# Performance work log

Measured on AMD Instinct MI355X. Metric: run time of the kernel, lower is better.

## Reference

```python
import jax, jax.numpy as jnp
import numpy as np

N = 50000
E = 1600000
D_IN, D_EMB, D_H, D_OUT, HEADS = 128, 128, 128, 64, 2


def setup_inputs() -> dict:
    key = jax.random.key(0)
    ks = jax.random.split(key, 12)
    return {
        "x": jax.random.normal(ks[0], (N, D_IN), jnp.float32),
        "edge_index": jax.random.randint(ks[1], (2, E), 0, N, dtype=jnp.int32),
        "node_indices": jnp.arange(N, dtype=jnp.int32),
        "emb": jax.random.normal(ks[2], (N, D_EMB), jnp.float32) * 0.1,
        "W_gcn": jax.random.normal(ks[3], (D_IN + D_EMB, D_H), jnp.float32) * 0.06,
        "b_gcn": jnp.zeros((D_H,), jnp.float32),
        "W_sage_l": jax.random.normal(ks[4], (D_H, D_H), jnp.float32) * 0.08,
        "W_sage_r": jax.random.normal(ks[5], (D_H, D_H), jnp.float32) * 0.08,
        "b_sage": jnp.zeros((D_H,), jnp.float32),
        "W_gat": jax.random.normal(ks[6], (D_H, HEADS, D_H), jnp.float32) * 0.08,
        "att_src": jax.random.normal(ks[7], (HEADS, D_H), jnp.float32) * 0.1,
        "att_dst": jax.random.normal(ks[8], (HEADS, D_H), jnp.float32) * 0.1,
        "b_gat": jnp.zeros((D_H,), jnp.float32),
        "W_out": jax.random.normal(ks[9], (D_H, D_OUT), jnp.float32) * 0.08,
        "b_out": jnp.zeros((D_OUT,), jnp.float32),
    }


def _forward(x, edge_index, node_indices, emb, W_gcn, b_gcn,
             W_sage_l, W_sage_r, b_sage, W_gat, att_src, att_dst, b_gat,
             W_out, b_out):
    n = x.shape[0]
    seg = jax.ops.segment_sum
    loops = jnp.arange(n, dtype=edge_index.dtype)

    # node2vec embedding lookup + concat
    h = jnp.concatenate([x, emb[node_indices]], axis=1)  # [N, D_IN+D_EMB]

    # --- GCNConv (symmetric norm, self loops) ---
    src = jnp.concatenate([edge_index[0], loops])
    dst = jnp.concatenate([edge_index[1], loops])
    deg = seg(jnp.ones_like(dst, jnp.float32), dst, num_segments=n)
    dinv = jnp.where(deg > 0, jax.lax.rsqrt(jnp.maximum(deg, 1.0)), 0.0)
    norm = dinv[src] * dinv[dst]                     # [E+N]
    hW = h @ W_gcn                                   # [N, D_H]
    h = seg(hW[src] * norm[:, None], dst, num_segments=n) + b_gcn
    h = jax.nn.relu(h)

    # --- SAGEConv (mean aggregation, no self loops) ---
    s, d = edge_index[0], edge_index[1]
    agg = seg(h[s], d, num_segments=n)
    cnt = seg(jnp.ones_like(d, jnp.float32), d, num_segments=n)
    mean = agg / jnp.maximum(cnt, 1.0)[:, None]
    h = mean @ W_sage_l + h @ W_sage_r + b_sage
    h = jax.nn.relu(h)

    # --- GATConv heads=2, concat=False (mean over heads), self loops ---
    xW = jnp.einsum('nd,dhc->nhc', h, W_gat)         # [N, H, D_H]
    a_src = jnp.einsum('nhc,hc->nh', xW, att_src)    # [N, H]
    a_dst = jnp.einsum('nhc,hc->nh', xW, att_dst)
    alpha = jax.nn.leaky_relu(a_src[src] + a_dst[dst], 0.2)  # [E+N, H]
    amax = jax.ops.segment_max(alpha, dst, num_segments=n)
    alpha = jnp.exp(alpha - amax[dst])
    asum = seg(alpha, dst, num_segments=n)
    alpha = alpha / (asum[dst] + 1e-16)
    out = seg(xW[src] * alpha[:, :, None], dst, num_segments=n)  # [N, H, D_H]
    h = jax.nn.relu(out.mean(axis=1) + b_gat)

    return h @ W_out + b_out


def reference(x, edge_index, node_indices, emb, W_gcn, b_gcn,
              W_sage_l, W_sage_r, b_sage, W_gat, att_src, att_dst, b_gat,
              W_out, b_out):
    return _forward(x, edge_index, node_indices, emb, W_gcn, b_gcn,
                    W_sage_l, W_sage_r, b_sage, W_gat, att_src, att_dst, b_gat,
                    W_out, b_out)
```

## Files before the change

### kernel.cpp

```cpp
#include <hip/hip_runtime.h>


typedef short bf16x8 __attribute__((ext_vector_type(8)));
typedef float f32x4  __attribute__((ext_vector_type(4)));

static __device__ __forceinline__ float leaky02(float x) {
    return x > 0.f ? x : 0.2f * x;
}
static __device__ __forceinline__ unsigned short f2bf(float f) {
    unsigned u = __float_as_uint(f);
    u = (u + 0x7FFFu + ((u >> 16) & 1u)) >> 16;
    return (unsigned short)u;
}
static __device__ __forceinline__ float bf2f(unsigned short h) {
    return __uint_as_float(((unsigned)h) << 16);
}
static __device__ __forceinline__ float4 bf4(ushort4 h) {
    return make_float4(bf2f(h.x), bf2f(h.y), bf2f(h.z), bf2f(h.w));
}
static __device__ __forceinline__ void split_bf(float v, unsigned short& h,
                                                unsigned short& l) {
    unsigned u = __float_as_uint(v);
    unsigned uh = u & 0xFFFF0000u;
    h = (unsigned short)(uh >> 16);
    l = f2bf(v - __uint_as_float(uh));
}

__global__ void deg_edges(const int* __restrict__ dst, int* __restrict__ degi, int E) {
    int e = blockIdx.x * blockDim.x + threadIdx.x;
    if (e < E) atomicAdd(&degi[dst[e]], 1);
}

__global__ __launch_bounds__(256)
void scan_part_norm(const int* __restrict__ degi, int* __restrict__ partial,
                    float* __restrict__ dinv, float* __restrict__ icnt, int n)
{
    int t = threadIdx.x;
    int base = blockIdx.x * 1024 + t * 4;
    int s = 0;
#pragma unroll
    for (int i = 0; i < 4; ++i) {
        int g = base + i;
        if (g < n) {
            int de = degi[g];
            s += de;
            dinv[g] = rsqrtf((float)(de + 1));
            icnt[g] = 1.0f / (float)(de > 1 ? de : 1);
        }
    }
#pragma unroll
    for (int m = 32; m > 0; m >>= 1) s += __shfl_xor(s, m, 64);
    __shared__ int wsum[4];
    if ((t & 63) == 0) wsum[t >> 6] = s;
    __syncthreads();
    if (t == 0) partial[blockIdx.x] = wsum[0] + wsum[1] + wsum[2] + wsum[3];
}

__global__ __launch_bounds__(64)
void scan_offsets(int* __restrict__ partial, int nb)
{
    int t = threadIdx.x;
    int carry = 0;
    for (int base = 0; base < nb; base += 64) {
        int i = base + t;
        int v = (i < nb) ? partial[i] : 0;
        int incl = v;
#pragma unroll
        for (int m = 1; m < 64; m <<= 1) {
            int o = __shfl_up(incl, m, 64);
            if (t >= m) incl += o;
        }
        if (i < nb) partial[i] = incl - v + carry;
        carry += __shfl(incl, 63, 64);
    }
}

__global__ __launch_bounds__(256)
void scan_write(const int* __restrict__ degi, const int* __restrict__ partial,
                int* __restrict__ rowptr, int n)
{
    __shared__ int tmp[256];
    int t = threadIdx.x;
    int base = blockIdx.x * 1024 + t * 4;
    int v[4]; int s = 0;
#pragma unroll
    for (int i = 0; i < 4; ++i) {
        int g = base + i;
        v[i] = (g < n) ? degi[g] : 0;
        s += v[i];
    }
    tmp[t] = s;
    __syncthreads();
    for (int off = 1; off < 256; off <<= 1) {
        int a = (t >= off) ? tmp[t - off] : 0;
        __syncthreads();
        tmp[t] += a;
        __syncthreads();
    }
    int run = tmp[t] - s + partial[blockIdx.x];
#pragma unroll
    for (int i = 0; i < 4; ++i) {
        int g = base + i;
        run += v[i];
        if (g < n) rowptr[g + 1] = run;
    }
    if (blockIdx.x == 0 && t == 0) rowptr[0] = 0;
}

__global__ void csr_fill(const int* __restrict__ src, const int* __restrict__ dst,
                         const int* __restrict__ rowptr, int* __restrict__ fill,
                         int* __restrict__ csr, int E)
{
    int e = blockIdx.x * blockDim.x + threadIdx.x;
    if (e >= E) return;
    int d = dst[e];
    int pos = rowptr[d] + atomicAdd(&fill[d], 1);
    csr[pos] = src[e];
}

template<bool HAS_A2, bool RELU, bool HAS_BIAS, bool HAS_IDX, bool SCALE,
         bool ATT, bool OUT_BF16>
__global__ __launch_bounds__(256)
void gemm_mfma(const float* __restrict__ A1, const float* __restrict__ W1,
               const float* __restrict__ A2, const float* __restrict__ W2,
               const int* __restrict__ idx2, const float* __restrict__ bias,
               const float* __restrict__ scale,
               const float* __restrict__ att_src, const float* __restrict__ att_dst,
               float* __restrict__ a_s, float* __restrict__ a_d,
               float* __restrict__ C, int nrows, int ncW, int ncC)
{
    __shared__ unsigned short ABh[8][65][8], ABl[8][65][8];
    __shared__ unsigned short WBh[8][65][8], WBl[8][65][8];
    const int t    = threadIdx.x;
    const int lane = t & 63;
    const int wv   = t >> 6;
    const int l15  = lane & 15;
    const int lg   = lane >> 4;
    const int row0 = blockIdx.x * 128;
    const int colOff = blockIdx.y * 128;

    f32x4 acc[2][8];
#pragma unroll
    for (int mt = 0; mt < 2; ++mt)
#pragma unroll
        for (int nt = 0; nt < 8; ++nt) acc[mt][nt] = (f32x4){0.f, 0.f, 0.f, 0.f};

    const int npass = HAS_A2 ? 2 : 1;
    for (int p = 0; p < npass; ++p) {
        const float* A = (p == 0) ? A1 : A2;
        const float* W = (p == 0) ? W1 : W2;
        for (int kt = 0; kt < 4; ++kt) {
#pragma unroll
            for (int i = 0; i < 4; ++i) {
                int f = i * 256 + t;
                int r = f >> 3, c4 = (f & 7) << 2;
                int row = row0 + r; if (row >= nrows) row = nrows - 1;
                int arow = (p == 1 && HAS_IDX) ? idx2[row] : row;
                float4 v = *(const float4*)(A + (size_t)arow * 128 + kt * 32 + c4);
                int rg = r >> 4;
                int slot = (r & 15) + ((c4 >> 3) << 4);
                int joff = c4 & 4;
                unsigned short h0,l0,h1,l1,h2,l2,h3,l3;
                split_bf(v.x, h0, l0); split_bf(v.y, h1, l1);
                split_bf(v.z, h2, l2); split_bf(v.w, h3, l3);
                *(ushort4*)&ABh[rg][slot][joff] = make_ushort4(h0, h1, h2, h3);
                *(ushort4*)&ABl[rg][slot][joff] = make_ushort4(l0, l1, l2, l3);
            }
#pragma unroll
            for (int i = 0; i < 4; ++i) {
                int f = i * 256 + t;
                int wr = f >> 5, wc4 = (f & 31) << 2;
                float4 v = *(const float4*)(W + (size_t)(kt * 32 + wr) * ncW + colOff + wc4);
                int jj = wr & 7, kg16 = (wr >> 3) << 4;
                int nt = wc4 >> 4, sb = (wc4 & 15) + kg16;
                unsigned short h, l;
                split_bf(v.x, h, l); WBh[nt][sb + 0][jj] = h; WBl[nt][sb + 0][jj] = l;
                split_bf(v.y, h, l); WBh[nt][sb + 1][jj] = h; WBl[nt][sb + 1][jj] = l;
                split_bf(v.z, h, l); WBh[nt][sb + 2][jj] = h; WBl[nt][sb + 2][jj] = l;
                split_bf(v.w, h, l); WBh[nt][sb + 3][jj] = h; WBl[nt][sb + 3][jj] = l;
            }
            __syncthreads();
            bf16x8 ah0 = *reinterpret_cast<const bf16x8*>(&ABh[wv * 2 + 0][lane][0]);
            bf16x8 al0 = *reinterpret_cast<const bf16x8*>(&ABl[wv * 2 + 0][lane][0]);
            bf16x8 ah1 = *reinterpret_cast<const bf16x8*>(&ABh[wv * 2 + 1][lane][0]);
            bf16x8 al1 = *reinterpret_cast<const bf16x8*>(&ABl[wv * 2 + 1][lane][0]);
#pragma unroll
            for (int nt = 0; nt < 8; ++nt) {
                bf16x8 bh = *reinterpret_cast<const bf16x8*>(&WBh[nt][lane][0]);
                bf16x8 bl = *reinterpret_cast<const bf16x8*>(&WBl[nt][lane][0]);
                acc[0][nt] = __builtin_amdgcn_mfma_f32_16x16x32_bf16(al0, bh, acc[0][nt], 0, 0, 0);
                acc[0][nt] = __builtin_amdgcn_mfma_f32_16x16x32_bf16(ah0, bl, acc[0][nt], 0, 0, 0);
                acc[0][nt] = __builtin_amdgcn_mfma_f32_16x16x32_bf16(ah0, bh, acc[0][nt], 0, 0, 0);
                acc[1][nt] = __builtin_amdgcn_mfma_f32_16x16x32_bf16(al1, bh, acc[1][nt], 0, 0, 0);
                acc[1][nt] = __builtin_amdgcn_mfma_f32_16x16x32_bf16(ah1, bl, acc[1][nt], 0, 0, 0);
                acc[1][nt] = __builtin_amdgcn_mfma_f32_16x16x32_bf16(ah1, bh, acc[1][nt], 0, 0, 0);
            }
            __syncthreads();
        }
    }

    float bias_v[8], as_v[8], ad_v[8];
#pragma unroll
    for (int nt = 0; nt < 8; ++nt) {
        int col = colOff + nt * 16 + l15;
        if (HAS_BIAS) bias_v[nt] = bias[col];
        if (ATT) { as_v[nt] = att_src[col]; ad_v[nt] = att_dst[col]; }
    }
#pragma unroll
    for (int mt = 0; mt < 2; ++mt) {
#pragma unroll
        for (int reg = 0; reg < 4; ++reg) {
            int row = row0 + wv * 32 + mt * 16 + lg * 4 + reg;
            bool ok = row < nrows;
            float sc = 1.f;
            if (SCALE) sc = ok ? scale[row] : 0.f;
            float vv[8];
            float ps = 0.f, pd = 0.f;
#pragma unroll
            for (int nt = 0; nt < 8; ++nt) {
                float v = acc[mt][nt][reg];
                if (SCALE) v *= sc;
                if (HAS_BIAS) v += bias_v[nt];
                if (RELU) v = fmaxf(v, 0.f);
                vv[nt] = v;
                if (ATT) { ps = fmaf(v, as_v[nt], ps); pd = fmaf(v, ad_v[nt], pd); }
            }
            if (ok) {
                if (OUT_BF16) {
                    unsigned short* cp =
                        (unsigned short*)C + (size_t)row * ncC + colOff + l15;
#pragma unroll
                    for (int nt = 0; nt < 8; ++nt) cp[nt * 16] = f2bf(vv[nt]);
                } else {
                    float* cp = C + (size_t)row * ncC + colOff + l15;
#pragma unroll
                    for (int nt = 0; nt < 8; ++nt) cp[nt * 16] = vv[nt];
                }
            }
            if (ATT) {
#pragma unroll
                for (int m = 1; m < 16; m <<= 1) {
                    ps += __shfl_xor(ps, m, 64);
                    pd += __shfl_xor(pd, m, 64);
                }
                if (ok && l15 == 0) {
                    a_s[row * 2 + blockIdx.y] = ps;
                    a_d[row * 2 + blockIdx.y] = pd;
                }
            }
        }
    }
}

__global__ __launch_bounds__(256)
void gcn_gather(const int* __restrict__ rowptr, const int* __restrict__ csr,
                const float* __restrict__ dinv,
                const unsigned short* __restrict__ hWb,
                const float* __restrict__ b, float* __restrict__ h1,
                unsigned short* __restrict__ h1b, int n)
{
    int d = blockIdx.x * 4 + (threadIdx.x >> 6);
    if (d >= n) return;
    int lane = threadIdx.x & 63;
    int half = lane >> 5;
    int c = (lane & 31) << 2;
    int r0 = rowptr[d], r1 = rowptr[d + 1];
    float4 acc = make_float4(0.f, 0.f, 0.f, 0.f);
    int j = r0 + half;
    for (; j + 6 < r1; j += 8) {
        int s0 = csr[j], s1 = csr[j + 2], s2 = csr[j + 4], s3 = csr[j + 6];
        float4 v0 = bf4(*(const ushort4*)(hWb + (size_t)s0 * 128 + c));
        float4 v1 = bf4(*(const ushort4*)(hWb + (size_t)s1 * 128 + c));
        float4 v2 = bf4(*(const ushort4*)(hWb + (size_t)s2 * 128 + c));
        float4 v3 = bf4(*(const ushort4*)(hWb + (size_t)s3 * 128 + c));
        acc.x += (v0.x + v1.x) + (v2.x + v3.x);
        acc.y += (v0.y + v1.y) + (v2.y + v3.y);
        acc.z += (v0.z + v1.z) + (v2.z + v3.z);
        acc.w += (v0.w + v1.w) + (v2.w + v3.w);
    }
    for (; j < r1; j += 2) {
        int s = csr[j];
        float4 v = bf4(*(const ushort4*)(hWb + (size_t)s * 128 + c));
        acc.x += v.x; acc.y += v.y; acc.z += v.z; acc.w += v.w;
    }
    acc.x += __shfl_xor(acc.x, 32, 64);
    acc.y += __shfl_xor(acc.y, 32, 64);
    acc.z += __shfl_xor(acc.z, 32, 64);
    acc.w += __shfl_xor(acc.w, 32, 64);
    if (lane < 32) {
        float dd = dinv[d];
        float4 vd = bf4(*(const ushort4*)(hWb + (size_t)d * 128 + c));
        float4 bb = *(const float4*)(b + c);
        float4 o;
        o.x = fmaxf(fmaf(acc.x + vd.x, dd, bb.x), 0.f);
        o.y = fmaxf(fmaf(acc.y + vd.y, dd, bb.y), 0.f);
        o.z = fmaxf(fmaf(acc.z + vd.z, dd, bb.z), 0.f);
        o.w = fmaxf(fmaf(acc.w + vd.w, dd, bb.w), 0.f);
        *(float4*)(h1 + (size_t)d * 128 + c) = o;
        ushort4 p;
        p.x = f2bf(o.x); p.y = f2bf(o.y); p.z = f2bf(o.z); p.w = f2bf(o.w);
        *(ushort4*)(h1b + (size_t)d * 128 + c) = p;
    }
}

__global__ __launch_bounds__(256)
void sage_gather(const int* __restrict__ rowptr, const int* __restrict__ csr,
                 const float* __restrict__ icnt,
                 const unsigned short* __restrict__ h1b,
                 float* __restrict__ mean, int n)
{
    int d = blockIdx.x * 4 + (threadIdx.x >> 6);
    if (d >= n) return;
    int lane = threadIdx.x & 63;
    int half = lane >> 5;
    int c = (lane & 31) << 2;
    int r0 = rowptr[d], r1 = rowptr[d + 1];
    float4 acc = make_float4(0.f, 0.f, 0.f, 0.f);
    int j = r0 + half;
    for (; j + 6 < r1; j += 8) {
        int s0 = csr[j], s1 = csr[j + 2], s2 = csr[j + 4], s3 = csr[j + 6];
        float4 v0 = bf4(*(const ushort4*)(h1b + (size_t)s0 * 128 + c));
        float4 v1 = bf4(*(const ushort4*)(h1b + (size_t)s1 * 128 + c));
        float4 v2 = bf4(*(const ushort4*)(h1b + (size_t)s2 * 128 + c));
        float4 v3 = bf4(*(const ushort4*)(h1b + (size_t)s3 * 128 + c));
        acc.x += (v0.x + v1.x) + (v2.x + v3.x);
        acc.y += (v0.y + v1.y) + (v2.y + v3.y);
        acc.z += (v0.z + v1.z) + (v2.z + v3.z);
        acc.w += (v0.w + v1.w) + (v2.w + v3.w);
    }
    for (; j < r1; j += 2) {
        int s = csr[j];
        float4 v = bf4(*(const ushort4*)(h1b + (size_t)s * 128 + c));
        acc.x += v.x; acc.y += v.y; acc.z += v.z; acc.w += v.w;
    }
    acc.x += __shfl_xor(acc.x, 32, 64);
    acc.y += __shfl_xor(acc.y, 32, 64);
    acc.z += __shfl_xor(acc.z, 32, 64);
    acc.w += __shfl_xor(acc.w, 32, 64);
    if (lane < 32) {
        float ic = icnt[d];
        float4 o;
        o.x = acc.x * ic; o.y = acc.y * ic; o.z = acc.z * ic; o.w = acc.w * ic;
        *(float4*)(mean + (size_t)d * 128 + c) = o;
    }
}

__global__ __launch_bounds__(256)
void gat_gather(const int* __restrict__ rowptr, const int* __restrict__ csr,
                const float* __restrict__ a_s, const float* __restrict__ a_d,
                const unsigned short* __restrict__ xWb,
                const float* __restrict__ b_gat,
                const float* __restrict__ W_out, const float* __restrict__ b_out,
                float* __restrict__ out, int n)
{
    __shared__ float h3row[4][128];
    int wv = threadIdx.x >> 6;
    int d = blockIdx.x * 4 + wv;
    if (d >= n) return;
    int lane = threadIdx.x & 63;
    const int hoff = lane >> 5;
    const int hsel = lane & 32;
    int r0 = rowptr[d], r1 = rowptr[d + 1];
    const int nE = r1 - r0;
    const float adh = a_d[d * 2 + hoff];

    float4 acc = make_float4(0.f, 0.f, 0.f, 0.f);
    float wacc = 0.f;

    for (int blk = 0; blk < nE; blk += 32) {
        int eidx = blk + (lane & 31);
        int s_l = d;
        float wl = 0.f;
        if (eidx < nE) {
            s_l = csr[r0 + eidx];
            wl = __expf(leaky02(a_s[s_l * 2 + hoff] + adh));
        }
        wacc += wl;
        int cnt = min(32, nE - blk);
        int e = 0;
        for (; e + 4 <= cnt; e += 4) {
            int   s0 = __shfl(s_l, e + 0, 64), s1 = __shfl(s_l, e + 1, 64);
            int   s2 = __shfl(s_l, e + 2, 64), s3 = __shfl(s_l, e + 3, 64);
            float w0 = __shfl(wl, (e + 0) | hsel, 64);
            float w1 = __shfl(wl, (e + 1) | hsel, 64);
            float w2 = __shfl(wl, (e + 2) | hsel, 64);
            float w3 = __shfl(wl, (e + 3) | hsel, 64);
            float4 v0 = bf4(((const ushort4*)(xWb + (size_t)s0 * 256))[lane]);
            float4 v1 = bf4(((const ushort4*)(xWb + (size_t)s1 * 256))[lane]);
            float4 v2 = bf4(((const ushort4*)(xWb + (size_t)s2 * 256))[lane]);
            float4 v3 = bf4(((const ushort4*)(xWb + (size_t)s3 * 256))[lane]);
            acc.x = fmaf(v0.x, w0, fmaf(v1.x, w1, fmaf(v2.x, w2, fmaf(v3.x, w3, acc.x))));
            acc.y = fmaf(v0.y, w0, fmaf(v1.y, w1, fmaf(v2.y, w2, fmaf(v3.y, w3, acc.y))));
            acc.z = fmaf(v0.z, w0, fmaf(v1.z, w1, fmaf(v2.z, w2, fmaf(v3.z, w3, acc.z))));
            acc.w = fmaf(v0.w, w0, fmaf(v1.w, w1, fmaf(v2.w, w2, fmaf(v3.w, w3, acc.w))));
        }
        for (; e < cnt; ++e) {
            int   s = __shfl(s_l, e, 64);
            float w = __shfl(wl, e | hsel, 64);
            float4 v = bf4(((const ushort4*)(xWb + (size_t)s * 256))[lane]);
            acc.x = fmaf(v.x, w, acc.x);
            acc.y = fmaf(v.y, w, acc.y);
            acc.z = fmaf(v.z, w, acc.z);
            acc.w = fmaf(v.w, w, acc.w);
        }
    }

    float wself = __expf(leaky02(a_s[d * 2 + hoff] + adh));
    {
        float4 v = bf4(((const ushort4*)(xWb + (size_t)d * 256))[lane]);
        acc.x = fmaf(v.x, wself, acc.x);
        acc.y = fmaf(v.y, wself, acc.y);
        acc.z = fmaf(v.z, wself, acc.z);
        acc.w = fmaf(v.w, wself, acc.w);
    }
#pragma unroll
    for (int sh = 16; sh > 0; sh >>= 1) wacc += __shfl_xor(wacc, sh, 64);
    float inv = 1.f / (wacc + wself + 1e-16f);
    acc.x *= inv; acc.y *= inv; acc.z *= inv; acc.w *= inv;

    float c0 = acc.x + __shfl_xor(acc.x, 32, 64);
    float c1 = acc.y + __shfl_xor(acc.y, 32, 64);
    float c2 = acc.z + __shfl_xor(acc.z, 32, 64);
    float c3 = acc.w + __shfl_xor(acc.w, 32, 64);
    if (lane < 32) {
        float4 bb = ((const float4*)b_gat)[lane];
        float4 o;
        o.x = fmaxf(0.5f * c0 + bb.x, 0.f);
        o.y = fmaxf(0.5f * c1 + bb.y, 0.f);
        o.z = fmaxf(0.5f * c2 + bb.z, 0.f);
        o.w = fmaxf(0.5f * c3 + bb.w, 0.f);
        ((float4*)h3row[wv])[lane] = o;
    }
    __threadfence_block();
    const float* hr = h3row[wv];
    float t0 = 0.f, t1 = 0.f, t2 = 0.f, t3 = 0.f;
#pragma unroll 8
    for (int k = 0; k < 128; k += 4) {
        t0 = fmaf(hr[k + 0], W_out[(k + 0) * 64 + lane], t0);
        t1 = fmaf(hr[k + 1], W_out[(k + 1) * 64 + lane], t1);
        t2 = fmaf(hr[k + 2], W_out[(k + 2) * 64 + lane], t2);
        t3 = fmaf(hr[k + 3], W_out[(k + 3) * 64 + lane], t3);
    }
    out[(size_t)d * 64 + lane] = (t0 + t1) + (t2 + t3) + b_out[lane];
}

extern "C" void kernel_launch(void* const* d_in, const int* in_sizes, int n_in,
                              void* d_out, int out_size, void* d_ws, size_t ws_size,
                              hipStream_t stream)
{
    const float* x      = (const float*)d_in[0];
    const int*   ei     = (const int*)d_in[1];
    const int*   nidx   = (const int*)d_in[2];
    const float* emb    = (const float*)d_in[3];
    const float* W_gcn  = (const float*)d_in[4];
    const float* b_gcn  = (const float*)d_in[5];
    const float* W_sl   = (const float*)d_in[6];
    const float* W_sr   = (const float*)d_in[7];
    const float* b_sage = (const float*)d_in[8];
    const float* W_gat  = (const float*)d_in[9];
    const float* att_s  = (const float*)d_in[10];
    const float* att_d  = (const float*)d_in[11];
    const float* b_gat  = (const float*)d_in[12];
    const float* W_out  = (const float*)d_in[13];
    const float* b_out  = (const float*)d_in[14];
    float* out = (float*)d_out;

    const int n = in_sizes[0] / 128;
    const int E = in_sizes[1] / 2;
    const int* esrc = ei;
    const int* edst = ei + E;

    const size_t P = (size_t)n * 128;
    const int nb_scan = (n + 1023) / 1024;
    float* ws   = (float*)d_ws;
    float* mean = ws;
    float* h1   = ws + P;
    float* h2   = ws + 2 * P;
    unsigned short* hWb = (unsigned short*)(ws + 3 * P);
    unsigned short* h1b = (unsigned short*)(ws + 3 * P + P / 2);
    unsigned short* xWb = (unsigned short*)(ws + 4 * P);
    float* dinv = ws + 5 * P;
    float* icnt = dinv + n;
    float* a_s  = icnt + n;
    float* a_d  = a_s + 2 * n;
    int* degi   = (int*)(a_d + 2 * n);
    int* fill   = degi + n;
    int* rowptr = fill + n;
    int* partial= rowptr + n + 1;
    int* csr    = partial + nb_scan + 1;

    const int TB = 256;
    int nblk_e     = (E + TB - 1) / TB;
    int nblk_wav_n = (n + 3) / 4;
    int gemm_rows  = (n + 127) / 128;

    hipMemsetAsync(degi, 0, 2 * (size_t)n * sizeof(int), stream);
    deg_edges<<<nblk_e, TB, 0, stream>>>(edst, degi, E);
    scan_part_norm<<<nb_scan, TB, 0, stream>>>(degi, partial, dinv, icnt, n);
    scan_offsets<<<1, 64, 0, stream>>>(partial, nb_scan);
    scan_write<<<nb_scan, TB, 0, stream>>>(degi, partial, rowptr, n);
    csr_fill<<<nblk_e, TB, 0, stream>>>(esrc, edst, rowptr, fill, csr, E);

    gemm_mfma<true, false, false, true, true, false, true>
        <<<dim3(gemm_rows, 1), TB, 0, stream>>>(
        x, W_gcn, emb, W_gcn + 128 * 128, nidx, nullptr, dinv,
        nullptr, nullptr, nullptr, nullptr, (float*)hWb, n, 128, 128);
    gcn_gather<<<nblk_wav_n, TB, 0, stream>>>(rowptr, csr, dinv, hWb, b_gcn,
                                              h1, h1b, n);

    sage_gather<<<nblk_wav_n, TB, 0, stream>>>(rowptr, csr, icnt, h1b, mean, n);
    gemm_mfma<true, true, true, false, false, false, false>
        <<<dim3(gemm_rows, 1), TB, 0, stream>>>(
        mean, W_sl, h1, W_sr, nullptr, b_sage, nullptr,
        nullptr, nullptr, nullptr, nullptr, h2, n, 128, 128);

    gemm_mfma<false, false, false, false, false, true, true>
        <<<dim3(gemm_rows, 2), TB, 0, stream>>>(
        h2, W_gat, nullptr, nullptr, nullptr, nullptr, nullptr,
        att_s, att_d, a_s, a_d, (float*)xWb, n, 256, 256);
    gat_gather<<<nblk_wav_n, TB, 0, stream>>>(rowptr, csr, a_s, a_d, xWb, b_gat,
                                              W_out, b_out, out, n);
}
```

Baseline: 604.8 us.

## Store intermediates in bf16, drop A low-part MFMAs, reuse rowptr as CSR fill counter

Intermediate activations (mean, h1, h2) are now stored only in bf16, and the GEMM loads bf16 A operands directly. The A-side low-half split is removed, so each tile issues 2 MFMAs instead of 3. The CSR fill now advances rowptr atomically in place of a separate fill array, and the gathers read row bounds from the shifted pointers. This cuts memory traffic, one memset and MFMA work, at the cost of lower precision on activation inputs to the GEMMs.

```diff
diff --git a/kernel.cpp b/kernel.cpp
--- a/kernel.cpp
+++ b/kernel.cpp
@@ -101,35 +101,33 @@
 #pragma unroll
     for (int i = 0; i < 4; ++i) {
         int g = base + i;
+        if (g < n) rowptr[g] = run;
         run += v[i];
-        if (g < n) rowptr[g + 1] = run;
-    }
-    if (blockIdx.x == 0 && t == 0) rowptr[0] = 0;
+    }
 }
 
 __global__ void csr_fill(const int* __restrict__ src, const int* __restrict__ dst,
-                         const int* __restrict__ rowptr, int* __restrict__ fill,
-                         int* __restrict__ csr, int E)
+                         int* __restrict__ rowptr, int* __restrict__ csr, int E)
 {
     int e = blockIdx.x * blockDim.x + threadIdx.x;
     if (e >= E) return;
     int d = dst[e];
-    int pos = rowptr[d] + atomicAdd(&fill[d], 1);
+    int pos = atomicAdd(&rowptr[d], 1);
     csr[pos] = src[e];
 }
 
 template<bool HAS_A2, bool RELU, bool HAS_BIAS, bool HAS_IDX, bool SCALE,
-         bool ATT, bool OUT_BF16>
+         bool ATT, bool OUT_BF16, bool A_BF16>
 __global__ __launch_bounds__(256)
-void gemm_mfma(const float* __restrict__ A1, const float* __restrict__ W1,
-               const float* __restrict__ A2, const float* __restrict__ W2,
+void gemm_mfma(const void* __restrict__ A1, const float* __restrict__ W1,
+               const void* __restrict__ A2, const float* __restrict__ W2,
                const int* __restrict__ idx2, const float* __restrict__ bias,
                const float* __restrict__ scale,
                const float* __restrict__ att_src, const float* __restrict__ att_dst,
                float* __restrict__ a_s, float* __restrict__ a_d,
                float* __restrict__ C, int nrows, int ncW, int ncC)
 {
-    __shared__ unsigned short ABh[8][65][8], ABl[8][65][8];
+    __shared__ unsigned short ABh[8][65][8];
     __shared__ unsigned short WBh[8][65][8], WBl[8][65][8];
     const int t    = threadIdx.x;
     const int lane = t & 63;
@@ -147,24 +145,33 @@
 
     const int npass = HAS_A2 ? 2 : 1;
     for (int p = 0; p < npass; ++p) {
-        const float* A = (p == 0) ? A1 : A2;
+        const void* A = (p == 0) ? A1 : A2;
         const float* W = (p == 0) ? W1 : W2;
         for (int kt = 0; kt < 4; ++kt) {
-#pragma unroll
-            for (int i = 0; i < 4; ++i) {
-                int f = i * 256 + t;
-                int r = f >> 3, c4 = (f & 7) << 2;
-                int row = row0 + r; if (row >= nrows) row = nrows - 1;
-                int arow = (p == 1 && HAS_IDX) ? idx2[row] : row;
-                float4 v = *(const float4*)(A + (size_t)arow * 128 + kt * 32 + c4);
-                int rg = r >> 4;
-                int slot = (r & 15) + ((c4 >> 3) << 4);
-                int joff = c4 & 4;
-                unsigned short h0,l0,h1,l1,h2,l2,h3,l3;
-                split_bf(v.x, h0, l0); split_bf(v.y, h1, l1);
-                split_bf(v.z, h2, l2); split_bf(v.w, h3, l3);
-                *(ushort4*)&ABh[rg][slot][joff] = make_ushort4(h0, h1, h2, h3);
-                *(ushort4*)&ABl[rg][slot][joff] = make_ushort4(l0, l1, l2, l3);
+            if (A_BF16) {
+                const unsigned short* Ab = (const unsigned short*)A;
+#pragma unroll
+                for (int i = 0; i < 2; ++i) {
+                    int f = i * 256 + t;
+                    int r = f >> 2, kq = f & 3;
+                    int row = row0 + r; if (row >= nrows) row = nrows - 1;
+                    int arow = (p == 1 && HAS_IDX) ? idx2[row] : row;
+                    bf16x8 v = *(const bf16x8*)(Ab + (size_t)arow * 128 + kt * 32 + kq * 8);
+                    *(bf16x8*)&ABh[r >> 4][(r & 15) + (kq << 4)][0] = v;
+                }
+            } else {
+                const float* Af = (const float*)A;
+#pragma unroll
+                for (int i = 0; i < 4; ++i) {
+                    int f = i * 256 + t;
+                    int r = f >> 3, c4 = (f & 7) << 2;
+                    int row = row0 + r; if (row >= nrows) row = nrows - 1;
+                    int arow = (p == 1 && HAS_IDX) ? idx2[row] : row;
+                    float4 v = *(const float4*)(Af + (size_t)arow * 128 + kt * 32 + c4);
+                    int slot = (r & 15) + ((c4 >> 3) << 4);
+                    *(ushort4*)&ABh[r >> 4][slot][c4 & 4] =
+                        make_ushort4(f2bf(v.x), f2bf(v.y), f2bf(v.z), f2bf(v.w));
+                }
             }
 #pragma unroll
             for (int i = 0; i < 4; ++i) {
@@ -180,20 +187,16 @@
                 split_bf(v.w, h, l); WBh[nt][sb + 3][jj] = h; WBl[nt][sb + 3][jj] = l;
             }
             __syncthreads();
-            bf16x8 ah0 = *reinterpret_cast<const bf16x8*>(&ABh[wv * 2 + 0][lane][0]);
-            bf16x8 al0 = *reinterpret_cast<const bf16x8*>(&ABl[wv * 2 + 0][lane][0]);
-            bf16x8 ah1 = *reinterpret_cast<const bf16x8*>(&ABh[wv * 2 + 1][lane][0]);
-            bf16x8 al1 = *reinterpret_cast<const bf16x8*>(&ABl[wv * 2 + 1][lane][0]);
+            bf16x8 a0 = *reinterpret_cast<const bf16x8*>(&ABh[wv * 2 + 0][lane][0]);
+            bf16x8 a1 = *reinterpret_cast<const bf16x8*>(&ABh[wv * 2 + 1][lane][0]);
 #pragma unroll
             for (int nt = 0; nt < 8; ++nt) {
                 bf16x8 bh = *reinterpret_cast<const bf16x8*>(&WBh[nt][lane][0]);
                 bf16x8 bl = *reinterpret_cast<const bf16x8*>(&WBl[nt][lane][0]);
-                acc[0][nt] = __builtin_amdgcn_mfma_f32_16x16x32_bf16(al0, bh, acc[0][nt], 0, 0, 0);
-                acc[0][nt] = __builtin_amdgcn_mfma_f32_16x16x32_bf16(ah0, bl, acc[0][nt], 0, 0, 0);
-                acc[0][nt] = __builtin_amdgcn_mfma_f32_16x16x32_bf16(ah0, bh, acc[0][nt], 0, 0, 0);
-                acc[1][nt] = __builtin_amdgcn_mfma_f32_16x16x32_bf16(al1, bh, acc[1][nt], 0, 0, 0);
-                acc[1][nt] = __builtin_amdgcn_mfma_f32_16x16x32_bf16(ah1, bl, acc[1][nt], 0, 0, 0);
-                acc[1][nt] = __builtin_amdgcn_mfma_f32_16x16x32_bf16(ah1, bh, acc[1][nt], 0, 0, 0);
+                acc[0][nt] = __builtin_amdgcn_mfma_f32_16x16x32_bf16(a0, bl, acc[0][nt], 0, 0, 0);
+                acc[0][nt] = __builtin_amdgcn_mfma_f32_16x16x32_bf16(a0, bh, acc[0][nt], 0, 0, 0);
+                acc[1][nt] = __builtin_amdgcn_mfma_f32_16x16x32_bf16(a1, bl, acc[1][nt], 0, 0, 0);
+                acc[1][nt] = __builtin_amdgcn_mfma_f32_16x16x32_bf16(a1, bh, acc[1][nt], 0, 0, 0);
             }
             __syncthreads();
         }
@@ -256,7 +259,7 @@
 void gcn_gather(const int* __restrict__ rowptr, const int* __restrict__ csr,
                 const float* __restrict__ dinv,
                 const unsigned short* __restrict__ hWb,
-                const float* __restrict__ b, float* __restrict__ h1,
+                const float* __restrict__ b,
                 unsigned short* __restrict__ h1b, int n)
 {
     int d = blockIdx.x * 4 + (threadIdx.x >> 6);
@@ -264,7 +267,8 @@
     int lane = threadIdx.x & 63;
     int half = lane >> 5;
     int c = (lane & 31) << 2;
-    int r0 = rowptr[d], r1 = rowptr[d + 1];
+    int r1 = rowptr[d];
+    int r0 = (d == 0) ? 0 : rowptr[d - 1];
     float4 acc = make_float4(0.f, 0.f, 0.f, 0.f);
     int j = r0 + half;
     for (; j + 6 < r1; j += 8) {
@@ -291,15 +295,12 @@
         float dd = dinv[d];
         float4 vd = bf4(*(const ushort4*)(hWb + (size_t)d * 128 + c));
         float4 bb = *(const float4*)(b + c);
-        float4 o;
-        o.x = fmaxf(fmaf(acc.x + vd.x, dd, bb.x), 0.f);
-        o.y = fmaxf(fmaf(acc.y + vd.y, dd, bb.y), 0.f);
-        o.z = fmaxf(fmaf(acc.z + vd.z, dd, bb.z), 0.f);
-        o.w = fmaxf(fmaf(acc.w + vd.w, dd, bb.w), 0.f);
-        *(float4*)(h1 + (size_t)d * 128 + c) = o;
-        ushort4 p;
-        p.x = f2bf(o.x); p.y = f2bf(o.y); p.z = f2bf(o.z); p.w = f2bf(o.w);
-        *(ushort4*)(h1b + (size_t)d * 128 + c) = p;
+        float o0 = fmaxf(fmaf(acc.x + vd.x, dd, bb.x), 0.f);
+        float o1 = fmaxf(fmaf(acc.y + vd.y, dd, bb.y), 0.f);
+        float o2 = fmaxf(fmaf(acc.z + vd.z, dd, bb.z), 0.f);
+        float o3 = fmaxf(fmaf(acc.w + vd.w, dd, bb.w), 0.f);
+        *(ushort4*)(h1b + (size_t)d * 128 + c) =
+            make_ushort4(f2bf(o0), f2bf(o1), f2bf(o2), f2bf(o3));
     }
 }
 
@@ -307,14 +308,15 @@
 void sage_gather(const int* __restrict__ rowptr, const int* __restrict__ csr,
                  const float* __restrict__ icnt,
                  const unsigned short* __restrict__ h1b,
-                 float* __restrict__ mean, int n)
+                 unsigned short* __restrict__ meanb, int n)
 {
     int d = blockIdx.x * 4 + (threadIdx.x >> 6);
     if (d >= n) return;
     int lane = threadIdx.x & 63;
     int half = lane >> 5;
     int c = (lane & 31) << 2;
-    int r0 = rowptr[d], r1 = rowptr[d + 1];
+    int r1 = rowptr[d];
+    int r0 = (d == 0) ? 0 : rowptr[d - 1];
     float4 acc = make_float4(0.f, 0.f, 0.f, 0.f);
     int j = r0 + half;
     for (; j + 6 < r1; j += 8) {
@@ -339,9 +341,9 @@
     acc.w += __shfl_xor(acc.w, 32, 64);
     if (lane < 32) {
         float ic = icnt[d];
-        float4 o;
-        o.x = acc.x * ic; o.y = acc.y * ic; o.z = acc.z * ic; o.w = acc.w * ic;
-        *(float4*)(mean + (size_t)d * 128 + c) = o;
+        *(ushort4*)(meanb + (size_t)d * 128 + c) =
+            make_ushort4(f2bf(acc.x * ic), f2bf(acc.y * ic),
+                         f2bf(acc.z * ic), f2bf(acc.w * ic));
     }
 }
 
@@ -360,7 +362,8 @@
     int lane = threadIdx.x & 63;
     const int hoff = lane >> 5;
     const int hsel = lane & 32;
-    int r0 = rowptr[d], r1 = rowptr[d + 1];
+    int r1 = rowptr[d];
+    int r0 = (d == 0) ? 0 : rowptr[d - 1];
     const int nE = r1 - r0;
     const float adh = a_d[d * 2 + hoff];
 
@@ -472,21 +475,19 @@
 
     const size_t P = (size_t)n * 128;
     const int nb_scan = (n + 1023) / 1024;
-    float* ws   = (float*)d_ws;
-    float* mean = ws;
-    float* h1   = ws + P;
-    float* h2   = ws + 2 * P;
-    unsigned short* hWb = (unsigned short*)(ws + 3 * P);
-    unsigned short* h1b = (unsigned short*)(ws + 3 * P + P / 2);
-    unsigned short* xWb = (unsigned short*)(ws + 4 * P);
-    float* dinv = ws + 5 * P;
+    float* ws = (float*)d_ws;
+    unsigned short* hWb   = (unsigned short*)ws;
+    unsigned short* h1b   = (unsigned short*)(ws + P / 2);
+    unsigned short* meanb = (unsigned short*)(ws + P);
+    unsigned short* h2b   = (unsigned short*)(ws + 3 * P / 2);
+    unsigned short* xWb   = (unsigned short*)(ws + 2 * P);
+    float* dinv = ws + 3 * P;
     float* icnt = dinv + n;
     float* a_s  = icnt + n;
     float* a_d  = a_s + 2 * n;
     int* degi   = (int*)(a_d + 2 * n);
-    int* fill   = degi + n;
-    int* rowptr = fill + n;
-    int* partial= rowptr + n + 1;
+    int* rowptr = degi + n;
+    int* partial= rowptr + n;
     int* csr    = partial + nb_scan + 1;
 
     const int TB = 256;
@@ -494,29 +495,29 @@
     int nblk_wav_n = (n + 3) / 4;
     int gemm_rows  = (n + 127) / 128;
 
-    hipMemsetAsync(degi, 0, 2 * (size_t)n * sizeof(int), stream);
+    hipMemsetAsync(degi, 0, (size_t)n * sizeof(int), stream);
     deg_edges<<<nblk_e, TB, 0, stream>>>(edst, degi, E);
     scan_part_norm<<<nb_scan, TB, 0, stream>>>(degi, partial, dinv, icnt, n);
     scan_offsets<<<1, 64, 0, stream>>>(partial, nb_scan);
     scan_write<<<nb_scan, TB, 0, stream>>>(degi, partial, rowptr, n);
-    csr_fill<<<nblk_e, TB, 0, stream>>>(esrc, edst, rowptr, fill, csr, E);
-
-    gemm_mfma<true, false, false, true, true, false, true>
+    csr_fill<<<nblk_e, TB, 0, stream>>>(esrc, edst, rowptr, csr, E);
+
+    gemm_mfma<true, false, false, true, true, false, true, false>
         <<<dim3(gemm_rows, 1), TB, 0, stream>>>(
         x, W_gcn, emb, W_gcn + 128 * 128, nidx, nullptr, dinv,
         nullptr, nullptr, nullptr, nullptr, (float*)hWb, n, 128, 128);
     gcn_gather<<<nblk_wav_n, TB, 0, stream>>>(rowptr, csr, dinv, hWb, b_gcn,
-                                              h1, h1b, n);
-
-    sage_gather<<<nblk_wav_n, TB, 0, stream>>>(rowptr, csr, icnt, h1b, mean, n);
-    gemm_mfma<true, true, true, false, false, false, false>
+                                              h1b, n);
+
+    sage_gather<<<nblk_wav_n, TB, 0, stream>>>(rowptr, csr, icnt, h1b, meanb, n);
+    gemm_mfma<true, true, true, false, false, false, true, true>
         <<<dim3(gemm_rows, 1), TB, 0, stream>>>(
-        mean, W_sl, h1, W_sr, nullptr, b_sage, nullptr,
-        nullptr, nullptr, nullptr, nullptr, h2, n, 128, 128);
-
-    gemm_mfma<false, false, false, false, false, true, true>
+        meanb, W_sl, h1b, W_sr, nullptr, b_sage, nullptr,
+        nullptr, nullptr, nullptr, nullptr, (float*)h2b, n, 128, 128);
+
+    gemm_mfma<false, false, false, false, false, true, true, true>
         <<<dim3(gemm_rows, 2), TB, 0, stream>>>(
-        h2, W_gat, nullptr, nullptr, nullptr, nullptr, nullptr,
+        h2b, W_gat, nullptr, nullptr, nullptr, nullptr, nullptr,
         att_s, att_d, a_s, a_d, (float*)xWb, n, 256, 256);
     gat_gather<<<nblk_wav_n, TB, 0, stream>>>(rowptr, csr, a_s, a_d, xWb, b_gat,
                                               W_out, b_out, out, n);
```

Result: slower. 631.1 us (+4.3%).
